# Optimization experiments

Measured on AMD Instinct MI355X. Metric: run time of the kernel, lower is better.

The kernel has to match this reference:

```python
import jax, jax.numpy as jnp
import numpy as np

B, N, M, D = 4, 16384, 4096, 64


def setup_inputs() -> dict:
    key = jax.random.key(0)
    k1, k2, k3 = jax.random.split(key, 3)
    pointcloud = jax.random.normal(k1, (B, N, 3), dtype=jnp.float32)
    keys = jax.random.normal(k2, (M, 3), dtype=jnp.float32)
    values = jax.random.normal(k3, (M, D), dtype=jnp.float32)
    return {"pointcloud": pointcloud, "keys": keys, "values": values}


def reference(pointcloud, keys, values):
    # Nearest-key quantization: argmin over squared L2 distances.
    # Expand ||p - k||^2 = ||p||^2 - 2 p.k + ||k||^2 (GEMM form; avoids the
    # (B,N,M,3) broadcasted diff tensor of the original).
    p_sq = jnp.sum(pointcloud * pointcloud, axis=-1, keepdims=True)      # (B,N,1)
    k_sq = jnp.sum(keys * keys, axis=-1)                                  # (M,)
    cross = jnp.einsum('bnc,mc->bnm', pointcloud, keys)                   # (B,N,M)
    d2 = p_sq - 2.0 * cross + k_sq[None, None, :]                         # (B,N,M)
    ids = jnp.argmin(d2, axis=-1)                                         # (B,N) int
    # Embedding lookup (get_features): gather rows of the value table.
    feats = values[ids]                                                   # (B,N,D)
    return feats, ids[..., None], pointcloud
```

## Files before the change

### kernel.cpp

```cpp
#include <hip/hip_runtime.h>

#pragma clang fp contract(off)

#define MM 4096
#define DD 64
#define BN 65536
#define FEATS_OFF 0
#define IDS_OFF (BN * DD)
#define PC_OFF (IDS_OFF + BN)

#define CC 16
#define PP 8
#define PPB 128
#define NPAIR (MM / 2)
#define KIT (MM / (2 * CC))

__global__ __launch_bounds__(256, 2)
void quant_embed_kernel(const float* __restrict__ pc,
                        const float* __restrict__ keys,
                        const float* __restrict__ values,
                        float* __restrict__ out)
{
#pragma clang fp contract(off)
    __shared__ float4 skA[NPAIR];
    __shared__ float4 skB[NPAIR];

    const int tid = threadIdx.x;

    #pragma unroll
    for (int i = 0; i < NPAIR / 256; ++i) {
        const int j = tid + i * 256;
        const float2 f0 = ((const float2*)keys)[3 * j + 0];
        const float2 f1 = ((const float2*)keys)[3 * j + 1];
        const float2 f2 = ((const float2*)keys)[3 * j + 2];
        const float ksq0 = ((f0.x * f0.x) + (f0.y * f0.y)) + (f1.x * f1.x);
        const float ksq1 = ((f1.y * f1.y) + (f2.x * f2.x)) + (f2.y * f2.y);
        skA[j] = make_float4(2.0f * f0.x, 2.0f * f1.y, 2.0f * f0.y, 2.0f * f2.x);
        skB[j] = make_float4(2.0f * f1.x, 2.0f * f2.y, ksq0, ksq1);
    }

    {
        const int base = blockIdx.x * (PPB * 3 / 4);
        if (tid < PPB * 3 / 4) {
            ((float4*)(out + PC_OFF))[base + tid] =
                ((const float4*)pc)[base + tid];
        }
    }

    const int c = tid & (CC - 1);
    const int g = tid >> 4;
    const int p0 = blockIdx.x * PPB + g * PP;

    float arr[24];
    {
        const float4* pcv = (const float4*)(pc + 3 * p0);
        #pragma unroll
        for (int i = 0; i < 6; ++i) ((float4*)arr)[i] = pcv[i];
    }
    float px[PP], py[PP], pz[PP], psq[PP], bd[PP];
    int bm[PP];
    #pragma unroll
    for (int i = 0; i < PP; ++i) {
        px[i] = arr[3 * i + 0];
        py[i] = arr[3 * i + 1];
        pz[i] = arr[3 * i + 2];
        psq[i] = ((px[i] * px[i]) + (py[i] * py[i])) + (pz[i] * pz[i]);
        bd[i] = 3.402823466e38f;
        bm[i] = 0;
    }

    __syncthreads();

    #pragma unroll 2
    for (int k = 0; k < KIT; ++k) {
        const int j = (k << 4) + c;
        const float4 A  = skA[j];
        const float4 Bv = skB[j];
        const int m0 = (k << 5) + (c << 1);
        const int m1 = m0 + 1;
        #pragma unroll
        for (int i = 0; i < PP; ++i) {
            const float ca = ((px[i] * A.x) + (py[i] * A.z)) + (pz[i] * Bv.x);
            const float da = (psq[i] - ca) + Bv.z;
            const bool lta = da < bd[i];
            bd[i] = lta ? da : bd[i];
            bm[i] = lta ? m0 : bm[i];
            const float cb = ((px[i] * A.y) + (py[i] * A.w)) + (pz[i] * Bv.y);
            const float db = (psq[i] - cb) + Bv.w;
            const bool ltb = db < bd[i];
            bd[i] = ltb ? db : bd[i];
            bm[i] = ltb ? m1 : bm[i];
        }
    }

    #pragma unroll
    for (int i = 0; i < PP; ++i) {
        float d = bd[i];
        int   m = bm[i];
        #pragma unroll
        for (int off = 1; off < CC; off <<= 1) {
            const float od = __shfl_xor(d, off);
            const int   om = __shfl_xor(m, off);
            if (od < d || (od == d && om < m)) { d = od; m = om; }
        }
        bm[i] = m;
    }

    #pragma unroll
    for (int i = 0; i < PP; ++i) {
        const float4* vrow = (const float4*)(values + (size_t)bm[i] * DD);
        ((float4*)(out + FEATS_OFF + (size_t)(p0 + i) * DD))[c] = vrow[c];
        if (c == 0) out[IDS_OFF + p0 + i] = (float)bm[i];
    }
}

extern "C" void kernel_launch(void* const* d_in, const int* in_sizes, int n_in,
                              void* d_out, int out_size, void* d_ws, size_t ws_size,
                              hipStream_t stream) {
    const float* pc     = (const float*)d_in[0];
    const float* keys   = (const float*)d_in[1];
    const float* values = (const float*)d_in[2];
    float* out = (float*)d_out;

    dim3 grid(BN / PPB);
    dim3 block(256);
    quant_embed_kernel<<<grid, block, 0, stream>>>(pc, keys, values, out);
}
```

Before: 125.8 us.

## Use packed FP32 distance math and split keys across 32 lanes per point group

Distance evaluation for each key pair now uses two-wide float vectors, so the compiler can emit packed FP32 multiply and add instructions and do roughly half the distance arithmetic instructions. The block grows to 512 threads and each point group is now served by 32 lanes instead of 16. Each lane scans half as many keys, and the shuffle reduction gains one extra step. Launch bounds ask for four blocks per CU, which limits registers per thread and risks spills. The feature gather switches to float2 to match the wider lane group.

```diff
diff --git a/kernel.cpp b/kernel.cpp
--- a/kernel.cpp
+++ b/kernel.cpp
@@ -1,6 +1,8 @@
 #include <hip/hip_runtime.h>
 
 #pragma clang fp contract(off)
+
+typedef float v2f __attribute__((ext_vector_type(2)));
 
 #define MM 4096
 #define DD 64
@@ -9,13 +11,14 @@
 #define IDS_OFF (BN * DD)
 #define PC_OFF (IDS_OFF + BN)
 
-#define CC 16
+#define BLK 512
+#define CC 32
 #define PP 8
 #define PPB 128
 #define NPAIR (MM / 2)
 #define KIT (MM / (2 * CC))
 
-__global__ __launch_bounds__(256, 2)
+__global__ __launch_bounds__(BLK, 4)
 void quant_embed_kernel(const float* __restrict__ pc,
                         const float* __restrict__ keys,
                         const float* __restrict__ values,
@@ -28,8 +31,8 @@
     const int tid = threadIdx.x;
 
     #pragma unroll
-    for (int i = 0; i < NPAIR / 256; ++i) {
-        const int j = tid + i * 256;
+    for (int i = 0; i < NPAIR / BLK; ++i) {
+        const int j = tid + i * BLK;
         const float2 f0 = ((const float2*)keys)[3 * j + 0];
         const float2 f1 = ((const float2*)keys)[3 * j + 1];
         const float2 f2 = ((const float2*)keys)[3 * j + 2];
@@ -48,7 +51,7 @@
     }
 
     const int c = tid & (CC - 1);
-    const int g = tid >> 4;
+    const int g = tid >> 5;
     const int p0 = blockIdx.x * PPB + g * PP;
 
     float arr[24];
@@ -73,20 +76,29 @@
 
     #pragma unroll 2
     for (int k = 0; k < KIT; ++k) {
-        const int j = (k << 4) + c;
+        const int j = (k << 5) + c;
         const float4 A  = skA[j];
         const float4 Bv = skB[j];
-        const int m0 = (k << 5) + (c << 1);
+        const v2f Kx = {A.x,  A.y};
+        const v2f Ky = {A.z,  A.w};
+        const v2f Kz = {Bv.x, Bv.y};
+        const v2f Ks = {Bv.z, Bv.w};
+        const int m0 = (k << 6) + (c << 1);
         const int m1 = m0 + 1;
         #pragma unroll
         for (int i = 0; i < PP; ++i) {
-            const float ca = ((px[i] * A.x) + (py[i] * A.z)) + (pz[i] * Bv.x);
-            const float da = (psq[i] - ca) + Bv.z;
+            const v2f tx = Kx * px[i];
+            const v2f ty = Ky * py[i];
+            const v2f tz = Kz * pz[i];
+            const v2f s  = tx + ty;
+            const v2f s2 = s + tz;
+            const v2f d  = psq[i] - s2;
+            const v2f d2 = d + Ks;
+            const float da = d2.x;
             const bool lta = da < bd[i];
             bd[i] = lta ? da : bd[i];
             bm[i] = lta ? m0 : bm[i];
-            const float cb = ((px[i] * A.y) + (py[i] * A.w)) + (pz[i] * Bv.y);
-            const float db = (psq[i] - cb) + Bv.w;
+            const float db = d2.y;
             const bool ltb = db < bd[i];
             bd[i] = ltb ? db : bd[i];
             bm[i] = ltb ? m1 : bm[i];
@@ -108,8 +120,8 @@
 
     #pragma unroll
     for (int i = 0; i < PP; ++i) {
-        const float4* vrow = (const float4*)(values + (size_t)bm[i] * DD);
-        ((float4*)(out + FEATS_OFF + (size_t)(p0 + i) * DD))[c] = vrow[c];
+        const float2* vrow = (const float2*)(values + (size_t)bm[i] * DD);
+        ((float2*)(out + FEATS_OFF + (size_t)(p0 + i) * DD))[c] = vrow[c];
         if (c == 0) out[IDS_OFF + p0 + i] = (float)bm[i];
     }
 }
@@ -123,6 +135,6 @@
     float* out = (float*)d_out;
 
     dim3 grid(BN / PPB);
-    dim3 block(256);
+    dim3 block(BLK);
     quant_embed_kernel<<<grid, block, 0, stream>>>(pc, keys, values, out);
 }
```

New measurement: 120.9 us. 3.9% less time.
